# Kernel optimization log

Hardware: AMD Instinct MI355X
Metric: run time of the kernel (lower is better)

## Reference

```python
import jax, jax.numpy as jnp
import numpy as np

B, L, DIM, H, HD = 2, 2048, 1024, 16, 64


def _rope_tables(L, hd):
    inv_freq = 1.0 / (10000.0 ** (np.arange(0, hd, 2, dtype=np.float32) / hd))
    t = np.arange(L, dtype=np.float32)
    freqs = np.outer(t, inv_freq)                 # [L, hd/2]
    emb = np.concatenate([freqs, freqs], axis=-1)  # [L, hd]
    return jnp.asarray(np.cos(emb)), jnp.asarray(np.sin(emb))


def setup_inputs() -> dict:
    key = jax.random.key(0)
    k1, k2, k3 = jax.random.split(key, 3)
    x = jax.random.normal(k1, (B, L, DIM), dtype=jnp.float32)
    cos, sin = _rope_tables(L, HD)
    w_qkv = jax.random.normal(k2, (DIM, 3 * H * HD), dtype=jnp.float32) * (DIM ** -0.5)
    w_out = jax.random.normal(k3, (H * HD, DIM), dtype=jnp.float32) * ((H * HD) ** -0.5)
    return {"x": x, "cos": cos, "sin": sin, "w_qkv": w_qkv, "w_out": w_out}


def _rotate_half(u):
    u1, u2 = jnp.split(u, 2, axis=-1)
    return jnp.concatenate([-u2, u1], axis=-1)


def _apply_rope(u, cos, sin):
    # u: [B, L, H, hd]; cos/sin: [L, hd]
    c = cos[None, :, None, :]
    s = sin[None, :, None, :]
    return u * c + _rotate_half(u) * s


def reference(x, cos, sin, w_qkv, w_out):
    b, l, _ = x.shape
    qkv = jnp.einsum('bld,de->ble', x, w_qkv).reshape(b, l, 3 * H, HD)
    q, k, v = jnp.split(qkv, 3, axis=2)          # each [B, L, H, hd]
    q = _apply_rope(q, cos, sin)
    k = _apply_rope(k, cos, sin)
    scale = HD ** -0.5                            # SDPA default scale
    scores = jnp.einsum('bqhd,bkhd->bhqk', q, k) * scale
    attn = jax.nn.softmax(scores, axis=-1)
    o = jnp.einsum('bhqk,bkhd->bqhd', attn, v).reshape(b, l, H * HD)
    return jnp.einsum('ble,ed->bld', o, w_out)
```

## Files before the change

### kernel.cpp

```cpp
#include <hip/hip_runtime.h>
#include <hip/hip_bf16.h>

#define BATCH 2
#define SEQ   2048
#define DIM   1024
#define NH    16
#define HD    64
#define K_DIM 1024

typedef __attribute__((ext_vector_type(8))) short short8;
typedef __attribute__((ext_vector_type(4))) short short4v;
typedef __attribute__((ext_vector_type(4))) float f32x4;
typedef unsigned short ushort_t;

__device__ __forceinline__ unsigned short f2b(float x) {
    unsigned int u = __float_as_uint(x);
    u += 0x7FFFu + ((u >> 16) & 1u);
    return (unsigned short)(u >> 16);
}

#define ASYNC_COPY16(gp, lp) \
    __builtin_amdgcn_global_load_lds((const __attribute__((address_space(1))) void*)(gp), \
                                     (__attribute__((address_space(3))) void*)(lp), 16, 0, 0)

__global__ __launch_bounds__(256)
void cast_bf16(const float* __restrict__ src, ushort_t* __restrict__ dst, int n4)
{
    int i = blockIdx.x * 256 + threadIdx.x;
    const int stride = gridDim.x * 256;
    for (; i < n4; i += stride) {
        float4 v = ((const float4*)src)[i];
        short4v o;
        o[0] = (short)f2b(v.x); o[1] = (short)f2b(v.y);
        o[2] = (short)f2b(v.z); o[3] = (short)f2b(v.w);
        ((short4v*)dst)[i] = o;
    }
}

__global__ __launch_bounds__(64)
void cast_transpose(const float* __restrict__ src, ushort_t* __restrict__ dst,
                    int K, int N)
{
    const int n  = blockIdx.x * 64 + threadIdx.x;
    const int k0 = blockIdx.y * 8;
    short8 o;
    #pragma unroll
    for (int j = 0; j < 8; ++j) o[j] = (short)f2b(src[(size_t)(k0 + j) * N + n]);
    *(short8*)(dst + (size_t)n * K + k0) = o;
}

__device__ __forceinline__ void mfma_gemm_tile(
    const ushort_t* __restrict__ Ag, const ushort_t* __restrict__ Bg,
    ushort_t* As, ushort_t* Bs, f32x4 acc[4][4])
{
    const int t = threadIdx.x;
    const int w = t >> 6, lane = t & 63;
    const int qd = lane >> 4, cl = lane & 15;
    const int srow = t >> 3;
    const int schunk = (t & 7) ^ (srow & 7);

    for (int k0 = 0; k0 < K_DIM; k0 += 64) {
        __syncthreads();
        #pragma unroll
        for (int j = 0; j < 4; ++j) {
            ASYNC_COPY16(Ag + (size_t)(j * 32 + srow) * K_DIM + k0 + schunk * 8,
                         As + (j * 32 + w * 8) * 64);
            ASYNC_COPY16(Bg + (size_t)(j * 32 + srow) * K_DIM + k0 + schunk * 8,
                         Bs + (j * 32 + w * 8) * 64);
        }
        __syncthreads();

        short8 af[4][2], bfr[4][2];
        #pragma unroll
        for (int rt = 0; rt < 4; ++rt) {
            const int row = (w >> 1) * 64 + rt * 16 + cl;
            #pragma unroll
            for (int kh = 0; kh < 2; ++kh)
                af[rt][kh] = *(const short8*)(As + row * 64 + (((kh * 4 + qd) ^ (row & 7)) * 8));
        }
        #pragma unroll
        for (int ct = 0; ct < 4; ++ct) {
            const int col = (w & 1) * 64 + ct * 16 + cl;
            #pragma unroll
            for (int kh = 0; kh < 2; ++kh)
                bfr[ct][kh] = *(const short8*)(Bs + col * 64 + (((kh * 4 + qd) ^ (col & 7)) * 8));
        }
        #pragma unroll
        for (int kh = 0; kh < 2; ++kh)
            #pragma unroll
            for (int rt = 0; rt < 4; ++rt)
                #pragma unroll
                for (int ct = 0; ct < 4; ++ct)
                    acc[rt][ct] = __builtin_amdgcn_mfma_f32_16x16x32_bf16(
                        af[rt][kh], bfr[ct][kh], acc[rt][ct], 0, 0, 0);
    }
}

__global__ __launch_bounds__(256)
void gemm_qkv_mfma(const ushort_t* __restrict__ xb, const ushort_t* __restrict__ wqb,
                   ushort_t* __restrict__ qb, ushort_t* __restrict__ kb,
                   ushort_t* __restrict__ vt,
                   const float* __restrict__ cosb, const float* __restrict__ sinb)
{
    __shared__ __align__(16) ushort_t As[128 * 64];
    __shared__ __align__(16) ushort_t Bs[128 * 64];
    const int m0 = blockIdx.y * 128, n0 = blockIdx.x * 128;

    f32x4 acc[4][4];
    #pragma unroll
    for (int i = 0; i < 4; ++i)
        #pragma unroll
        for (int j = 0; j < 4; ++j)
            #pragma unroll
            for (int r = 0; r < 4; ++r) acc[i][j][r] = 0.f;

    mfma_gemm_tile(xb + (size_t)m0 * K_DIM, wqb + (size_t)n0 * K_DIM, As, Bs, acc);

    const int t = threadIdx.x, w = t >> 6, lane = t & 63;
    const int qd = lane >> 4, cl = lane & 15;
    const int b = m0 >> 11;
    const int lbase = (m0 & 2047) + (w >> 1) * 64;
    const int region = blockIdx.x >> 3;
    const int h = (blockIdx.x & 7) * 2 + (w & 1);

    if (region < 2) {
        ushort_t* dst = region ? kb : qb;
        const float sc = region ? 1.0f : 0.18033688011111234f;
        #pragma unroll
        for (int rt = 0; rt < 4; ++rt) {
            #pragma unroll
            for (int r = 0; r < 4; ++r) {
                const int l = lbase + rt * 16 + qd * 4 + r;
                const float c0 = cosb[l * HD + cl],      s0 = sinb[l * HD + cl];
                const float c1 = cosb[l * HD + 16 + cl], s1 = sinb[l * HD + 16 + cl];
                const float v0 = acc[rt][0][r] * c0 - acc[rt][2][r] * s0;
                const float v1 = acc[rt][1][r] * c1 - acc[rt][3][r] * s1;
                const float v2 = acc[rt][2][r] * c0 + acc[rt][0][r] * s0;
                const float v3 = acc[rt][3][r] * c1 + acc[rt][1][r] * s1;
                ushort_t* p = dst + (((size_t)b * NH + h) * SEQ + l) * HD;
                p[cl]      = f2b(v0 * sc);
                p[16 + cl] = f2b(v1 * sc);
                p[32 + cl] = f2b(v2 * sc);
                p[48 + cl] = f2b(v3 * sc);
            }
        }
    } else {
        #pragma unroll
        for (int rt = 0; rt < 4; ++rt)
            #pragma unroll
            for (int ct = 0; ct < 4; ++ct) {
                const int d = ct * 16 + cl;
                const int l = lbase + rt * 16 + qd * 4;
                short4v o4;
                #pragma unroll
                for (int r = 0; r < 4; ++r) o4[r] = (short)f2b(acc[rt][ct][r]);
                *(short4v*)(vt + (((size_t)b * NH + h) * HD + d) * SEQ + l) = o4;
            }
    }
}

__global__ __launch_bounds__(256)
void gemm_out_mfma(const ushort_t* __restrict__ ob, const ushort_t* __restrict__ wob,
                   float* __restrict__ out)
{
    __shared__ __align__(16) ushort_t As[128 * 64];
    __shared__ __align__(16) ushort_t Bs[128 * 64];
    const int m0 = blockIdx.y * 128, n0 = blockIdx.x * 128;

    f32x4 acc[4][4];
    #pragma unroll
    for (int i = 0; i < 4; ++i)
        #pragma unroll
        for (int j = 0; j < 4; ++j)
            #pragma unroll
            for (int r = 0; r < 4; ++r) acc[i][j][r] = 0.f;

    mfma_gemm_tile(ob + (size_t)m0 * K_DIM, wob + (size_t)n0 * K_DIM, As, Bs, acc);

    const int t = threadIdx.x, w = t >> 6, lane = t & 63;
    const int qd = lane >> 4, cl = lane & 15;
    const int mbase = m0 + (w >> 1) * 64, nbase = n0 + (w & 1) * 64;
    #pragma unroll
    for (int rt = 0; rt < 4; ++rt)
        #pragma unroll
        for (int ct = 0; ct < 4; ++ct)
            #pragma unroll
            for (int r = 0; r < 4; ++r)
                out[(size_t)(mbase + rt * 16 + qd * 4 + r) * DIM + nbase + ct * 16 + cl] =
                    acc[rt][ct][r];
}

__global__ __launch_bounds__(256, 2)
void attn_mfma(const ushort_t* __restrict__ qb, const ushort_t* __restrict__ kb,
               const ushort_t* __restrict__ vt, ushort_t* __restrict__ o)
{
    const int qt = blockIdx.x, h = blockIdx.y, b = blockIdx.z;
    const int t = threadIdx.x;
    const int w = t >> 6, lane = t & 63;
    const int qd = lane >> 4, cl = lane & 15;
    constexpr int NT = SEQ / 64;

    __shared__ __align__(16) ushort_t Ks[2][64 * 64];
    __shared__ __align__(16) ushort_t Vs[2][64 * 64];
    __shared__ __align__(16) ushort_t P[4][2048];
    char* Pb = (char*)P[w];

    const size_t bh = (size_t)b * NH + h;
    const ushort_t* qbase = qb + (bh * SEQ + qt * 128 + w * 32) * HD;
    const ushort_t* kbase = kb + bh * SEQ * HD;
    const ushort_t* vbase = vt + bh * (size_t)HD * SEQ;

    const int p0 = w * 128 + lane;
    const int r0a = p0 >> 3,        c0a = (p0 & 7) ^ (r0a & 7);
    const int p1 = p0 + 64;
    const int r1a = p1 >> 3,        c1a = (p1 & 7) ^ (r1a & 7);
    const int ldsoff0 = (w * 128) * 8;
    const int ldsoff1 = (w * 128 + 64) * 8;

    short8 qf[2][2];
    #pragma unroll
    for (int nt = 0; nt < 2; ++nt)
        #pragma unroll
        for (int kh = 0; kh < 2; ++kh)
            qf[nt][kh] = *(const short8*)(qbase + (nt * 16 + cl) * HD + kh * 32 + qd * 8);

    f32x4 oaccT[4][2];
    float l_part[2] = {0.f, 0.f};
    #pragma unroll
    for (int dt = 0; dt < 4; ++dt)
        #pragma unroll
        for (int nt = 0; nt < 2; ++nt)
            #pragma unroll
            for (int r = 0; r < 4; ++r) oaccT[dt][nt][r] = 0.f;

    {
        const int kt = 0;
        ASYNC_COPY16(kbase + (size_t)(kt * 64 + r0a) * HD + c0a * 8, (ushort_t*)Ks[0] + ldsoff0);
        ASYNC_COPY16(kbase + (size_t)(kt * 64 + r1a) * HD + c1a * 8, (ushort_t*)Ks[0] + ldsoff1);
        ASYNC_COPY16(vbase + (size_t)r0a * SEQ + kt * 64 + c0a * 8,  (ushort_t*)Vs[0] + ldsoff0);
        ASYNC_COPY16(vbase + (size_t)r1a * SEQ + kt * 64 + c1a * 8,  (ushort_t*)Vs[0] + ldsoff1);
    }

    for (int kt = 0; kt < NT; ++kt) {
        const int cur = kt & 1;
        __syncthreads();

        if (kt + 1 < NT) {
            const int nx = kt + 1;
            ASYNC_COPY16(kbase + (size_t)(nx * 64 + r0a) * HD + c0a * 8, (ushort_t*)Ks[cur ^ 1] + ldsoff0);
            ASYNC_COPY16(kbase + (size_t)(nx * 64 + r1a) * HD + c1a * 8, (ushort_t*)Ks[cur ^ 1] + ldsoff1);
            ASYNC_COPY16(vbase + (size_t)r0a * SEQ + nx * 64 + c0a * 8,  (ushort_t*)Vs[cur ^ 1] + ldsoff0);
            ASYNC_COPY16(vbase + (size_t)r1a * SEQ + nx * 64 + c1a * 8,  (ushort_t*)Vs[cur ^ 1] + ldsoff1);
        }

        short8 kf[4][2], vf[4][2];
        #pragma unroll
        for (int mt = 0; mt < 4; ++mt)
            #pragma unroll
            for (int kh = 0; kh < 2; ++kh)
                kf[mt][kh] = *(const short8*)(Ks[cur] + ((mt * 16 + cl) * 8 + ((kh * 4 + qd) ^ (cl & 7))) * 8);
        #pragma unroll
        for (int dt = 0; dt < 4; ++dt)
            #pragma unroll
            for (int kh = 0; kh < 2; ++kh)
                vf[dt][kh] = *(const short8*)(Vs[cur] + ((dt * 16 + cl) * 8 + ((kh * 4 + qd) ^ (cl & 7))) * 8);

        f32x4 s[4][2];
        #pragma unroll
        for (int mt = 0; mt < 4; ++mt)
            #pragma unroll
            for (int nt = 0; nt < 2; ++nt)
                #pragma unroll
                for (int r = 0; r < 4; ++r) s[mt][nt][r] = 0.f;
        #pragma unroll
        for (int kh = 0; kh < 2; ++kh)
            #pragma unroll
            for (int mt = 0; mt < 4; ++mt)
                #pragma unroll
                for (int nt = 0; nt < 2; ++nt)
                    s[mt][nt] = __builtin_amdgcn_mfma_f32_16x16x32_bf16(
                        kf[mt][kh], qf[nt][kh], s[mt][nt], 0, 0, 0);

        #pragma unroll
        for (int nt = 0; nt < 2; ++nt) {
            #pragma unroll
            for (int mt = 0; mt < 4; ++mt) {
                const float e0 = __builtin_amdgcn_exp2f(s[mt][nt][0]);
                const float e1 = __builtin_amdgcn_exp2f(s[mt][nt][1]);
                const float e2 = __builtin_amdgcn_exp2f(s[mt][nt][2]);
                const float e3 = __builtin_amdgcn_exp2f(s[mt][nt][3]);
                l_part[nt] += (e0 + e1) + (e2 + e3);
                union { __hip_bfloat162 h2[2]; unsigned long long u64; } pk;
                pk.h2[0] = __float22bfloat162_rn(make_float2(e0, e1));
                pk.h2[1] = __float22bfloat162_rn(make_float2(e2, e3));
                const int g = (mt * 2 + (qd >> 1)) ^ (cl & 7);
                *(unsigned long long*)(Pb + (nt * 16 + cl) * 128 + g * 16 + (qd & 1) * 8) = pk.u64;
            }
        }
        __builtin_amdgcn_wave_barrier();

        short8 pf[2][2];
        #pragma unroll
        for (int nt = 0; nt < 2; ++nt)
            #pragma unroll
            for (int kh = 0; kh < 2; ++kh)
                pf[nt][kh] = *(const short8*)(Pb + (nt * 16 + cl) * 128 + (((kh * 4 + qd) ^ (cl & 7)) * 16));
        #pragma unroll
        for (int kh = 0; kh < 2; ++kh)
            #pragma unroll
            for (int dt = 0; dt < 4; ++dt)
                #pragma unroll
                for (int nt = 0; nt < 2; ++nt)
                    oaccT[dt][nt] = __builtin_amdgcn_mfma_f32_16x16x32_bf16(
                        vf[dt][kh], pf[nt][kh], oaccT[dt][nt], 0, 0, 0);
        __builtin_amdgcn_wave_barrier();
    }

    #pragma unroll
    for (int nt = 0; nt < 2; ++nt) {
        float l = l_part[nt];
        l += __shfl_xor(l, 16);
        l += __shfl_xor(l, 32);
        const float inv = 1.0f / l;
        const int query = qt * 128 + w * 32 + nt * 16 + cl;
        ushort_t* op = o + ((size_t)b * SEQ + query) * DIM + h * HD;
        #pragma unroll
        for (int dt = 0; dt < 4; ++dt) {
            short4v o4;
            #pragma unroll
            for (int r = 0; r < 4; ++r) o4[r] = (short)f2b(oaccT[dt][nt][r] * inv);
            *(short4v*)(op + dt * 16 + qd * 4) = o4;
        }
    }
}

extern "C" void kernel_launch(void* const* d_in, const int* in_sizes, int n_in,
                              void* d_out, int out_size, void* d_ws, size_t ws_size,
                              hipStream_t stream)
{
    const float* x     = (const float*)d_in[0];
    const float* cosb  = (const float*)d_in[1];
    const float* sinb  = (const float*)d_in[2];
    const float* w_qkv = (const float*)d_in[3];
    const float* w_out = (const float*)d_in[4];
    float* out = (float*)d_out;

    constexpr size_t XN  = (size_t)BATCH * SEQ * DIM;
    constexpr size_t QKN = (size_t)BATCH * NH * SEQ * HD;
    ushort_t* xb  = (ushort_t*)d_ws;
    ushort_t* wqb = xb  + XN;
    ushort_t* wob = wqb + (size_t)3072 * 1024;
    ushort_t* qb  = wob + (size_t)1024 * 1024;
    ushort_t* kb  = qb + QKN;
    ushort_t* vt  = kb + QKN;
    ushort_t* ob  = vt + QKN;

    cast_bf16<<<1024, 256, 0, stream>>>(x, xb, (int)(XN / 4));
    cast_transpose<<<dim3(48, 128), 64, 0, stream>>>(w_qkv, wqb, 1024, 3072);
    cast_transpose<<<dim3(16, 128), 64, 0, stream>>>(w_out, wob, 1024, 1024);

    gemm_qkv_mfma<<<dim3(24, 32), 256, 0, stream>>>(xb, wqb, qb, kb, vt, cosb, sinb);
    attn_mfma<<<dim3(SEQ / 128, NH, BATCH), 256, 0, stream>>>(qb, kb, vt, ob);
    gemm_out_mfma<<<dim3(8, 32), 256, 0, stream>>>(ob, wob, out);
}
```

Measured before the change: 213.5 us.

## Split attention over key halves, software-pipeline PV, double-buffer GEMM K-tiles

```diff
diff --git a/kernel.cpp b/kernel.cpp
--- a/kernel.cpp
+++ b/kernel.cpp
@@ -49,61 +49,64 @@
     *(short8*)(dst + (size_t)n * K + k0) = o;
 }
 
+__device__ __forceinline__ void gemm_stage(const ushort_t* __restrict__ Ag,
+                                           const ushort_t* __restrict__ Bg,
+                                           ushort_t* As, ushort_t* Bs,
+                                           int k0, int w, int r0, int c0)
+{
+    ASYNC_COPY16(Ag + (size_t)r0 * K_DIM + k0 + c0 * 8,        As + w * 512);
+    ASYNC_COPY16(Ag + (size_t)(64 + r0) * K_DIM + k0 + c0 * 8, As + w * 512 + 2048);
+    ASYNC_COPY16(Bg + (size_t)r0 * K_DIM + k0 + c0 * 8,        Bs + w * 512);
+    ASYNC_COPY16(Bg + (size_t)(64 + r0) * K_DIM + k0 + c0 * 8, Bs + w * 512 + 2048);
+}
+
 __device__ __forceinline__ void mfma_gemm_tile(
     const ushort_t* __restrict__ Ag, const ushort_t* __restrict__ Bg,
-    ushort_t* As, ushort_t* Bs, f32x4 acc[4][4])
+    ushort_t (&As)[2][128 * 32], ushort_t (&Bs)[2][128 * 32], f32x4 acc[4][4])
 {
     const int t = threadIdx.x;
     const int w = t >> 6, lane = t & 63;
     const int qd = lane >> 4, cl = lane & 15;
-    const int srow = t >> 3;
-    const int schunk = (t & 7) ^ (srow & 7);
-
-    for (int k0 = 0; k0 < K_DIM; k0 += 64) {
+    const int p0 = w * 64 + lane;
+    const int r0 = p0 >> 2;
+    const int c0 = (p0 & 3) ^ (r0 & 3);
+
+    gemm_stage(Ag, Bg, As[0], Bs[0], 0, w, r0, c0);
+
+    for (int kt = 0; kt < K_DIM / 32; ++kt) {
+        const int cur = kt & 1;
         __syncthreads();
-        #pragma unroll
-        for (int j = 0; j < 4; ++j) {
-            ASYNC_COPY16(Ag + (size_t)(j * 32 + srow) * K_DIM + k0 + schunk * 8,
-                         As + (j * 32 + w * 8) * 64);
-            ASYNC_COPY16(Bg + (size_t)(j * 32 + srow) * K_DIM + k0 + schunk * 8,
-                         Bs + (j * 32 + w * 8) * 64);
-        }
-        __syncthreads();
-
-        short8 af[4][2], bfr[4][2];
+        if (kt + 1 < K_DIM / 32)
+            gemm_stage(Ag, Bg, As[cur ^ 1], Bs[cur ^ 1], (kt + 1) * 32, w, r0, c0);
+
+        short8 af[4], bfr[4];
         #pragma unroll
         for (int rt = 0; rt < 4; ++rt) {
             const int row = (w >> 1) * 64 + rt * 16 + cl;
-            #pragma unroll
-            for (int kh = 0; kh < 2; ++kh)
-                af[rt][kh] = *(const short8*)(As + row * 64 + (((kh * 4 + qd) ^ (row & 7)) * 8));
+            af[rt] = *(const short8*)(As[cur] + row * 32 + ((qd ^ (row & 3)) * 8));
         }
         #pragma unroll
         for (int ct = 0; ct < 4; ++ct) {
             const int col = (w & 1) * 64 + ct * 16 + cl;
-            #pragma unroll
-            for (int kh = 0; kh < 2; ++kh)
-                bfr[ct][kh] = *(const short8*)(Bs + col * 64 + (((kh * 4 + qd) ^ (col & 7)) * 8));
+            bfr[ct] = *(const short8*)(Bs[cur] + col * 32 + ((qd ^ (col & 3)) * 8));
         }
         #pragma unroll
-        for (int kh = 0; kh < 2; ++kh)
-            #pragma unroll
-            for (int rt = 0; rt < 4; ++rt)
-                #pragma unroll
-                for (int ct = 0; ct < 4; ++ct)
-                    acc[rt][ct] = __builtin_amdgcn_mfma_f32_16x16x32_bf16(
-                        af[rt][kh], bfr[ct][kh], acc[rt][ct], 0, 0, 0);
-    }
-}
-
-__global__ __launch_bounds__(256)
+        for (int rt = 0; rt < 4; ++rt)
+            #pragma unroll
+            for (int ct = 0; ct < 4; ++ct)
+                acc[rt][ct] = __builtin_amdgcn_mfma_f32_16x16x32_bf16(
+                    af[rt], bfr[ct], acc[rt][ct], 0, 0, 0);
+    }
+}
+
+__global__ __launch_bounds__(256, 3)
 void gemm_qkv_mfma(const ushort_t* __restrict__ xb, const ushort_t* __restrict__ wqb,
                    ushort_t* __restrict__ qb, ushort_t* __restrict__ kb,
                    ushort_t* __restrict__ vt,
                    const float* __restrict__ cosb, const float* __restrict__ sinb)
 {
-    __shared__ __align__(16) ushort_t As[128 * 64];
-    __shared__ __align__(16) ushort_t Bs[128 * 64];
+    __shared__ __align__(16) ushort_t As[2][128 * 32];
+    __shared__ __align__(16) ushort_t Bs[2][128 * 32];
     const int m0 = blockIdx.y * 128, n0 = blockIdx.x * 128;
 
     f32x4 acc[4][4];
@@ -159,12 +162,12 @@
     }
 }
 
-__global__ __launch_bounds__(256)
+__global__ __launch_bounds__(256, 3)
 void gemm_out_mfma(const ushort_t* __restrict__ ob, const ushort_t* __restrict__ wob,
                    float* __restrict__ out)
 {
-    __shared__ __align__(16) ushort_t As[128 * 64];
-    __shared__ __align__(16) ushort_t Bs[128 * 64];
+    __shared__ __align__(16) ushort_t As[2][128 * 32];
+    __shared__ __align__(16) ushort_t Bs[2][128 * 32];
     const int m0 = blockIdx.y * 128, n0 = blockIdx.x * 128;
 
     f32x4 acc[4][4];
@@ -190,15 +193,19 @@
                     acc[rt][ct][r];
 }
 
-__global__ __launch_bounds__(256, 2)
+__global__ __launch_bounds__(256, 3)
 void attn_mfma(const ushort_t* __restrict__ qb, const ushort_t* __restrict__ kb,
-               const ushort_t* __restrict__ vt, ushort_t* __restrict__ o)
-{
-    const int qt = blockIdx.x, h = blockIdx.y, b = blockIdx.z;
+               const ushort_t* __restrict__ vt, float* __restrict__ Op,
+               float* __restrict__ lp)
+{
+    const int h = blockIdx.x;
+    const int b = blockIdx.y >> 1;
+    const int half = blockIdx.y & 1;
+    const int qt = blockIdx.z;
     const int t = threadIdx.x;
     const int w = t >> 6, lane = t & 63;
     const int qd = lane >> 4, cl = lane & 15;
-    constexpr int NT = SEQ / 64;
+    constexpr int NT = SEQ / 64 / 2;
 
     __shared__ __align__(16) ushort_t Ks[2][64 * 64];
     __shared__ __align__(16) ushort_t Vs[2][64 * 64];
@@ -211,9 +218,9 @@
     const ushort_t* vbase = vt + bh * (size_t)HD * SEQ;
 
     const int p0 = w * 128 + lane;
-    const int r0a = p0 >> 3,        c0a = (p0 & 7) ^ (r0a & 7);
+    const int r0a = p0 >> 3,  c0a = (p0 & 7) ^ (r0a & 7);
     const int p1 = p0 + 64;
-    const int r1a = p1 >> 3,        c1a = (p1 & 7) ^ (r1a & 7);
+    const int r1a = p1 >> 3,  c1a = (p1 & 7) ^ (r1a & 7);
     const int ldsoff0 = (w * 128) * 8;
     const int ldsoff1 = (w * 128 + 64) * 8;
 
@@ -233,24 +240,37 @@
             #pragma unroll
             for (int r = 0; r < 4; ++r) oaccT[dt][nt][r] = 0.f;
 
+    short8 pf_prev[2][2], vf_prev[4][2];
+    #pragma unroll
+    for (int nt = 0; nt < 2; ++nt)
+        #pragma unroll
+        for (int kh = 0; kh < 2; ++kh)
+            #pragma unroll
+            for (int e = 0; e < 8; ++e) pf_prev[nt][kh][e] = 0;
+    #pragma unroll
+    for (int dt = 0; dt < 4; ++dt)
+        #pragma unroll
+        for (int kh = 0; kh < 2; ++kh)
+            #pragma unroll
+            for (int e = 0; e < 8; ++e) vf_prev[dt][kh][e] = 0;
+
+    const int g0 = half * NT;
     {
-        const int kt = 0;
-        ASYNC_COPY16(kbase + (size_t)(kt * 64 + r0a) * HD + c0a * 8, (ushort_t*)Ks[0] + ldsoff0);
-        ASYNC_COPY16(kbase + (size_t)(kt * 64 + r1a) * HD + c1a * 8, (ushort_t*)Ks[0] + ldsoff1);
-        ASYNC_COPY16(vbase + (size_t)r0a * SEQ + kt * 64 + c0a * 8,  (ushort_t*)Vs[0] + ldsoff0);
-        ASYNC_COPY16(vbase + (size_t)r1a * SEQ + kt * 64 + c1a * 8,  (ushort_t*)Vs[0] + ldsoff1);
+        ASYNC_COPY16(kbase + (size_t)(g0 * 64 + r0a) * HD + c0a * 8, (ushort_t*)Ks[0] + ldsoff0);
+        ASYNC_COPY16(kbase + (size_t)(g0 * 64 + r1a) * HD + c1a * 8, (ushort_t*)Ks[0] + ldsoff1);
+        ASYNC_COPY16(vbase + (size_t)r0a * SEQ + g0 * 64 + c0a * 8,  (ushort_t*)Vs[0] + ldsoff0);
+        ASYNC_COPY16(vbase + (size_t)r1a * SEQ + g0 * 64 + c1a * 8,  (ushort_t*)Vs[0] + ldsoff1);
     }
 
     for (int kt = 0; kt < NT; ++kt) {
         const int cur = kt & 1;
         __syncthreads();
-
         if (kt + 1 < NT) {
-            const int nx = kt + 1;
-            ASYNC_COPY16(kbase + (size_t)(nx * 64 + r0a) * HD + c0a * 8, (ushort_t*)Ks[cur ^ 1] + ldsoff0);
-            ASYNC_COPY16(kbase + (size_t)(nx * 64 + r1a) * HD + c1a * 8, (ushort_t*)Ks[cur ^ 1] + ldsoff1);
-            ASYNC_COPY16(vbase + (size_t)r0a * SEQ + nx * 64 + c0a * 8,  (ushort_t*)Vs[cur ^ 1] + ldsoff0);
-            ASYNC_COPY16(vbase + (size_t)r1a * SEQ + nx * 64 + c1a * 8,  (ushort_t*)Vs[cur ^ 1] + ldsoff1);
+            const int g = g0 + kt + 1;
+            ASYNC_COPY16(kbase + (size_t)(g * 64 + r0a) * HD + c0a * 8, (ushort_t*)Ks[cur ^ 1] + ldsoff0);
+            ASYNC_COPY16(kbase + (size_t)(g * 64 + r1a) * HD + c1a * 8, (ushort_t*)Ks[cur ^ 1] + ldsoff1);
+            ASYNC_COPY16(vbase + (size_t)r0a * SEQ + g * 64 + c0a * 8,  (ushort_t*)Vs[cur ^ 1] + ldsoff0);
+            ASYNC_COPY16(vbase + (size_t)r1a * SEQ + g * 64 + c1a * 8,  (ushort_t*)Vs[cur ^ 1] + ldsoff1);
         }
 
         short8 kf[4][2], vf[4][2];
@@ -280,6 +300,15 @@
                 for (int nt = 0; nt < 2; ++nt)
                     s[mt][nt] = __builtin_amdgcn_mfma_f32_16x16x32_bf16(
                         kf[mt][kh], qf[nt][kh], s[mt][nt], 0, 0, 0);
+
+        #pragma unroll
+        for (int kh = 0; kh < 2; ++kh)
+            #pragma unroll
+            for (int dt = 0; dt < 4; ++dt)
+                #pragma unroll
+                for (int nt = 0; nt < 2; ++nt)
+                    oaccT[dt][nt] = __builtin_amdgcn_mfma_f32_16x16x32_bf16(
+                        vf_prev[dt][kh], pf_prev[nt][kh], oaccT[dt][nt], 0, 0, 0);
 
         #pragma unroll
         for (int nt = 0; nt < 2; ++nt) {
@@ -299,39 +328,65 @@
         }
         __builtin_amdgcn_wave_barrier();
 
-        short8 pf[2][2];
         #pragma unroll
         for (int nt = 0; nt < 2; ++nt)
             #pragma unroll
             for (int kh = 0; kh < 2; ++kh)
-                pf[nt][kh] = *(const short8*)(Pb + (nt * 16 + cl) * 128 + (((kh * 4 + qd) ^ (cl & 7)) * 16));
-        #pragma unroll
-        for (int kh = 0; kh < 2; ++kh)
-            #pragma unroll
-            for (int dt = 0; dt < 4; ++dt)
-                #pragma unroll
-                for (int nt = 0; nt < 2; ++nt)
-                    oaccT[dt][nt] = __builtin_amdgcn_mfma_f32_16x16x32_bf16(
-                        vf[dt][kh], pf[nt][kh], oaccT[dt][nt], 0, 0, 0);
-        __builtin_amdgcn_wave_barrier();
-    }
+                pf_prev[nt][kh] = *(const short8*)(Pb + (nt * 16 + cl) * 128 + (((kh * 4 + qd) ^ (cl & 7)) * 16));
+        #pragma unroll
+        for (int dt = 0; dt < 4; ++dt)
+            #pragma unroll
+            for (int kh = 0; kh < 2; ++kh)
+                vf_prev[dt][kh] = vf[dt][kh];
+    }
+
+    #pragma unroll
+    for (int kh = 0; kh < 2; ++kh)
+        #pragma unroll
+        for (int dt = 0; dt < 4; ++dt)
+            #pragma unroll
+            for (int nt = 0; nt < 2; ++nt)
+                oaccT[dt][nt] = __builtin_amdgcn_mfma_f32_16x16x32_bf16(
+                    vf_prev[dt][kh], pf_prev[nt][kh], oaccT[dt][nt], 0, 0, 0);
 
     #pragma unroll
     for (int nt = 0; nt < 2; ++nt) {
         float l = l_part[nt];
         l += __shfl_xor(l, 16);
         l += __shfl_xor(l, 32);
-        const float inv = 1.0f / l;
         const int query = qt * 128 + w * 32 + nt * 16 + cl;
-        ushort_t* op = o + ((size_t)b * SEQ + query) * DIM + h * HD;
-        #pragma unroll
-        for (int dt = 0; dt < 4; ++dt) {
-            short4v o4;
-            #pragma unroll
-            for (int r = 0; r < 4; ++r) o4[r] = (short)f2b(oaccT[dt][nt][r] * inv);
-            *(short4v*)(op + dt * 16 + qd * 4) = o4;
-        }
-    }
+        if (qd == 0)
+            lp[((size_t)half * BATCH + b) * NH * SEQ + ((size_t)h) * SEQ + query
+               + (size_t)b * 0] = l;
+        float* op = Op + (((size_t)half * BATCH + b) * SEQ + query) * DIM + h * HD;
+        #pragma unroll
+        for (int dt = 0; dt < 4; ++dt)
+            *(f32x4*)(op + dt * 16 + qd * 4) = oaccT[dt][nt];
+    }
+}
+
+__global__ __launch_bounds__(256)
+void reduce_o(const float* __restrict__ Op, const float* __restrict__ lp,
+              ushort_t* __restrict__ ob)
+{
+    const int idx = blockIdx.x * 256 + threadIdx.x;
+    const int d4 = idx & 255;
+    const int l  = (idx >> 8) & 2047;
+    const int b  = idx >> 19;
+    const int h  = d4 >> 4;
+
+    const size_t o_off = ((size_t)b * SEQ + l) * DIM + d4 * 4;
+    const float4 a = *(const float4*)(Op + o_off);
+    const float4 c = *(const float4*)(Op + (size_t)BATCH * SEQ * DIM + o_off);
+    const size_t l_off = ((size_t)b * NH + h) * SEQ + l;
+    const float inv = 1.0f / (lp[l_off] + lp[(size_t)BATCH * NH * SEQ + l_off]);
+
+    short4v o4;
+    o4[0] = (short)f2b((a.x + c.x) * inv);
+    o4[1] = (short)f2b((a.y + c.y) * inv);
+    o4[2] = (short)f2b((a.z + c.z) * inv);
+    o4[3] = (short)f2b((a.w + c.w) * inv);
+    *(short4v*)(ob + o_off) = o4;
 }
 
 extern "C" void kernel_launch(void* const* d_in, const int* in_sizes, int n_in,
@@ -345,21 +400,26 @@
     const float* w_out = (const float*)d_in[4];
     float* out = (float*)d_out;
 
-    constexpr size_t XN  = (size_t)BATCH * SEQ * DIM;
-    constexpr size_t QKN = (size_t)BATCH * NH * SEQ * HD;
-    ushort_t* xb  = (ushort_t*)d_ws;
-    ushort_t* wqb = xb  + XN;
-    ushort_t* wob = wqb + (size_t)3072 * 1024;
-    ushort_t* qb  = wob + (size_t)1024 * 1024;
-    ushort_t* kb  = qb + QKN;
-    ushort_t* vt  = kb + QKN;
-    ushort_t* ob  = vt + QKN;
+    constexpr size_t MB = 1u << 20;
+    char* ws = (char*)d_ws;
+    ushort_t* qb  = (ushort_t*)(ws);
+    ushort_t* kb  = (ushort_t*)(ws + 8 * MB);
+    ushort_t* vt  = (ushort_t*)(ws + 16 * MB);
+    ushort_t* wob = (ushort_t*)(ws + 24 * MB);
+    float*    lp  = (float*)   (ws + 26 * MB);
+    float*    Op  = (float*)   (ws + 27 * MB);
+    ushort_t* xb  = (ushort_t*)(ws + 27 * MB);
+    ushort_t* wqb = (ushort_t*)(ws + 35 * MB);
+    ushort_t* ob  = qb;
+
+    constexpr size_t XN = (size_t)BATCH * SEQ * DIM;
 
     cast_bf16<<<1024, 256, 0, stream>>>(x, xb, (int)(XN / 4));
     cast_transpose<<<dim3(48, 128), 64, 0, stream>>>(w_qkv, wqb, 1024, 3072);
     cast_transpose<<<dim3(16, 128), 64, 0, stream>>>(w_out, wob, 1024, 1024);
 
     gemm_qkv_mfma<<<dim3(24, 32), 256, 0, stream>>>(xb, wqb, qb, kb, vt, cosb, sinb);
-    attn_mfma<<<dim3(SEQ / 128, NH, BATCH), 256, 0, stream>>>(qb, kb, vt, ob);
+    attn_mfma<<<dim3(16, 4, 16), 256, 0, stream>>>(qb, kb, vt, Op, lp);
+    reduce_o<<<4096, 256, 0, stream>>>(Op, lp, ob);
     gemm_out_mfma<<<dim3(8, 32), 256, 0, stream>>>(ob, wob, out);
 }
```

Result: no change. 209.6 us (-1.8%).
